# Kernel optimization log

Hardware: AMD Instinct MI355X
Metric: run time of the kernel (lower is better)

## Reference

```python
import jax, jax.numpy as jnp
import numpy as np


def setup_inputs() -> dict:
    key = jax.random.key(0)
    ks = jax.random.split(key, 6)
    B, S, D = 2048, 50, 128
    H, L = 8, 128
    return {
        "x": jax.random.normal(ks[0], (B, S, D), dtype=jnp.float32),
        "Wq": jax.random.normal(ks[1], (H, D, L), dtype=jnp.float32),
        "Wk": jax.random.normal(ks[2], (H, D, L), dtype=jnp.float32),
        "Wv": jax.random.normal(ks[3], (H, D, L), dtype=jnp.float32),
        "Ws": jax.random.normal(ks[4], (H, L), dtype=jnp.float32),
        "O": jax.random.normal(ks[5], (H * L, D), dtype=jnp.float32),
    }


def reference(x, Wq, Wk, Wv, Ws, O):
    # x: [B, S, D]; origin is the first node of each walk.
    B, S, D = x.shape
    H, _, L = Wq.shape
    origin = x[:, 0, :]  # [B, D]
    # key projection of origin is constant over the sequence -> compute once.
    k = jax.nn.sigmoid(jnp.einsum("bd,hdl->bhl", origin, Wk))  # [B, H, L]
    q = jax.nn.sigmoid(jnp.einsum("bsd,hdl->bshl", x, Wq))      # [B, S, H, L]
    v = jax.nn.sigmoid(jnp.einsum("bsd,hdl->bshl", x, Wv))      # [B, S, H, L]
    edge = k[:, None, :, :] * q                                  # [B, S, H, L]
    score = jnp.einsum("bshl,hl->bsh", edge, Ws)                 # [B, S, H]
    attn = jax.nn.softmax(score, axis=1)                         # softmax over walk positions
    res = jnp.einsum("bsh,bshl->bhl", attn, v)                   # [B, H, L]
    res = res.reshape(B, H * L)                                  # head-major concat (matches tf.concat)
    out = jax.nn.sigmoid(res @ O) + origin                       # [B, D]
    return out
```

## Files before the change

### kernel.cpp

```cpp
#include <hip/hip_runtime.h>
#include <hip/hip_bf16.h>


typedef _Float16 f16x8 __attribute__((ext_vector_type(8)));
typedef float f32x4 __attribute__((ext_vector_type(4)));

#define LOG2E 1.44269504088896340736f

__device__ __forceinline__ unsigned short f2h(float f) {
  _Float16 h = (_Float16)f;
  return __builtin_bit_cast(unsigned short, h);
}
__device__ __forceinline__ float h2f(unsigned short s) {
  return (float)__builtin_bit_cast(_Float16, s);
}
__device__ __forceinline__ float fexp2(float x) {
#if __has_builtin(__builtin_amdgcn_exp2f)
  return __builtin_amdgcn_exp2f(x);
#else
  return exp2f(x);
#endif
}
__device__ __forceinline__ float frcp(float x) {
#if __has_builtin(__builtin_amdgcn_rcpf)
  return __builtin_amdgcn_rcpf(x);
#else
  return 1.0f / x;
#endif
}
__device__ __forceinline__ float sig_scaled(float a) {
  return frcp(1.0f + fexp2(a));
}

__device__ __forceinline__ void dma16(const void* g, void* l) {
  __builtin_amdgcn_global_load_lds(
      (const __attribute__((address_space(1))) unsigned int*)g,
      (__attribute__((address_space(3))) unsigned int*)(unsigned int)(unsigned long long)l,
      16, 0, 0);
}

__global__ void prep_kernel(const float* __restrict__ Wq, const float* __restrict__ Wk,
                            const float* __restrict__ Wv, const float* __restrict__ O,
                            unsigned short* __restrict__ ws16) {
  const float NS = -LOG2E;
  int tid = blockIdx.x * 256 + threadIdx.x;
  for (int j = tid; j < 4 * 131072; j += 512 * 256) {
    int which = j >> 17;
    int i = j & 131071;
    float val;
    if (which == 0 || which == 2) {
      const float* W = (which == 0) ? Wq : Wv;
      int tau = i >> 11;
      int op = (i & 2047) * 2;
      int c = op >> 8;
      int o = op ^ ((c & 7) << 4);
      int k = (o & 255) >> 1;
      int n = tau * 16 + c;
      int h = n >> 7, lidx = n & 127;
      val = W[h * 16384 + k * 128 + lidx];
    } else if (which == 1) {
      int n = i >> 7, d = i & 127;
      int h = n >> 7, lidx = n & 127;
      val = Wk[h * 16384 + d * 128 + lidx];
    } else {
      int n = i >> 10, k = i & 1023;
      val = O[k * 128 + n];
    }
    ws16[j] = f2h(val * NS);
  }
}

__global__ __launch_bounds__(256, 2) void kw_kernel(
    const float* __restrict__ x, const float* __restrict__ Ws,
    const unsigned short* __restrict__ WkT, unsigned short* __restrict__ kw_all) {
  __shared__ __align__(16) char lds[8192];
  const int tid = threadIdx.x;
  const int b0 = blockIdx.x * 32;
  for (int i = tid; i < 1024; i += 256) {
    int row = i >> 5, c4 = i & 31;
    const float4 v = *(const float4*)(x + (size_t)(b0 + row) * 6400 + c4 * 4);
    uint2 pk;
    pk.x = (unsigned)f2h(v.x) | ((unsigned)f2h(v.y) << 16);
    pk.y = (unsigned)f2h(v.z) | ((unsigned)f2h(v.w) << 16);
    *(uint2*)(lds + row * 256 + ((c4 * 8) ^ ((row & 7) << 4))) = pk;
  }
  __syncthreads();
  const int w = tid >> 6, l = tid & 63, l15 = l & 15, l4 = l >> 4;
  f16x8 af[2][4];
#pragma unroll
  for (int mt = 0; mt < 2; ++mt)
#pragma unroll
    for (int kt = 0; kt < 4; ++kt) {
      int row = mt * 16 + l15;
      int c = kt * 64 + l4 * 16;
      af[mt][kt] = *(const f16x8*)(lds + row * 256 + (c ^ ((row & 7) << 4)));
    }
  const f16x8* B8 = (const f16x8*)WkT;
  for (int nt = 0; nt < 4; ++nt) {
    const int n0 = blockIdx.y * 256 + w * 64 + nt * 16;
    f16x8 bfr[4];
#pragma unroll
    for (int kt = 0; kt < 4; ++kt) bfr[kt] = B8[(size_t)(n0 + l15) * 16 + kt * 4 + l4];
    f32x4 acc[2];
#pragma unroll
    for (int mt = 0; mt < 2; ++mt) acc[mt] = (f32x4){0.f, 0.f, 0.f, 0.f};
#pragma unroll
    for (int mt = 0; mt < 2; ++mt)
#pragma unroll
      for (int kt = 0; kt < 4; ++kt)
        acc[mt] = __builtin_amdgcn_mfma_f32_16x16x32_f16(af[mt][kt], bfr[kt], acc[mt], 0, 0, 0);
    const float wsv = Ws[n0 + l15];
#pragma unroll
    for (int mt = 0; mt < 2; ++mt)
#pragma unroll
      for (int r = 0; r < 4; ++r) {
        int row = b0 + mt * 16 + l4 * 4 + r;
        kw_all[(size_t)row * 1024 + n0 + l15] = f2h(sig_scaled(acc[mt][r]) * wsv);
      }
  }
}

__global__ __launch_bounds__(256, 3) void fused_kernel(
    const float* __restrict__ x,
    const unsigned short* __restrict__ WqS, const unsigned short* __restrict__ WvS,
    const unsigned short* __restrict__ kw_all, unsigned short* __restrict__ res_all) {
  __shared__ __align__(16) char lds[49152];
  const int tid = threadIdx.x;
  const int b = blockIdx.x;
  const int w = tid >> 6, l = tid & 63, l15 = l & 15, l4 = l >> 4;
  const int ncol = w * 256;

  unsigned short kwr[16];
  {
    const unsigned short* kwp = kw_all + (size_t)b * 1024 + ncol + l15;
#pragma unroll
    for (int nt = 0; nt < 16; ++nt) kwr[nt] = kwp[nt * 16];
  }

  const float* xb = x + (size_t)b * 6400;
#pragma unroll
  for (int j = 0; j < 8; ++j) {
    int idx = tid + j * 256;
    int row = idx >> 5, c4 = idx & 31;
    uint2 pk = {0u, 0u};
    if (row < 50) {
      const float4 v = *(const float4*)(xb + row * 128 + c4 * 4);
      pk.x = (unsigned)f2h(v.x) | ((unsigned)f2h(v.y) << 16);
      pk.y = (unsigned)f2h(v.z) | ((unsigned)f2h(v.w) << 16);
    }
    *(uint2*)(lds + row * 256 + ((c4 * 8) ^ ((row & 7) << 4))) = pk;
  }
  __syncthreads();

  f16x8 af[4][4];
#pragma unroll
  for (int mt = 0; mt < 4; ++mt)
#pragma unroll
    for (int kt = 0; kt < 4; ++kt) {
      int row = mt * 16 + l15;
      int c = kt * 64 + l4 * 16;
      af[mt][kt] = *(const f16x8*)(lds + row * 256 + (c ^ ((row & 7) << 4)));
    }
  float kwf[16];
#pragma unroll
  for (int nt = 0; nt < 16; ++nt) kwf[nt] = h2f(kwr[nt]);
  __syncthreads();

  char* slotb = lds + w * 12288;

  {
    const char* s0 = (const char*)WqS + (size_t)(ncol >> 4) * 4096 + l * 16;
    dma16(s0, slotb);
    dma16(s0 + 1024, slotb + 1024);
    dma16(s0 + 2048, slotb + 2048);
    dma16(s0 + 3072, slotb + 3072);
    const char* s1 = s0 + 4096;
    char* n1 = slotb + 4096;
    dma16(s1, n1);
    dma16(s1 + 1024, n1 + 1024);
    dma16(s1 + 2048, n1 + 2048);
    dma16(s1 + 3072, n1 + 3072);
  }

  float pa[4][4];
#pragma unroll
  for (int mt = 0; mt < 4; ++mt)
#pragma unroll
    for (int r = 0; r < 4; ++r) pa[mt][r] = 0.f;

#pragma unroll
  for (int t = 0; t < 32; ++t) {
    const int nt = (t & 7) + ((t >> 4) << 3);
    char* cslot = slotb + (t % 3) * 4096;
    if (t < 30) {
      const int t2 = t + 2;
      const int nt2 = (t2 & 7) + ((t2 >> 4) << 3);
      const unsigned short* W2 = ((t2 >> 3) & 1) ? WvS : WqS;
      const char* s = (const char*)W2 + (size_t)((ncol >> 4) + nt2) * 4096 + l * 16;
      char* nslot = slotb + (t2 % 3) * 4096;
      dma16(s, nslot);
      dma16(s + 1024, nslot + 1024);
      dma16(s + 2048, nslot + 2048);
      dma16(s + 3072, nslot + 3072);
      asm volatile("s_waitcnt vmcnt(8)" ::: "memory");
    } else if (t == 30) {
      asm volatile("s_waitcnt vmcnt(4)" ::: "memory");
    } else {
      asm volatile("s_waitcnt vmcnt(0)" ::: "memory");
    }
    __builtin_amdgcn_s_setprio(1);
    f32x4 acc[4];
#pragma unroll
    for (int mt = 0; mt < 4; ++mt) acc[mt] = (f32x4){0.f, 0.f, 0.f, 0.f};
    {
      f16x8 bf0, bf1;
      {
        int o0 = (l15 * 256 + 0 * 64 + l4 * 16) ^ ((l15 & 7) << 4);
        int o1 = (l15 * 256 + 1 * 64 + l4 * 16) ^ ((l15 & 7) << 4);
        bf0 = *(const f16x8*)(cslot + o0);
        bf1 = *(const f16x8*)(cslot + o1);
      }
#pragma unroll
      for (int mt = 0; mt < 4; ++mt)
        acc[mt] = __builtin_amdgcn_mfma_f32_16x16x32_f16(af[mt][0], bf0, acc[mt], 0, 0, 0);
#pragma unroll
      for (int mt = 0; mt < 4; ++mt)
        acc[mt] = __builtin_amdgcn_mfma_f32_16x16x32_f16(af[mt][1], bf1, acc[mt], 0, 0, 0);
      {
        int o2 = (l15 * 256 + 2 * 64 + l4 * 16) ^ ((l15 & 7) << 4);
        int o3 = (l15 * 256 + 3 * 64 + l4 * 16) ^ ((l15 & 7) << 4);
        bf0 = *(const f16x8*)(cslot + o2);
        bf1 = *(const f16x8*)(cslot + o3);
      }
#pragma unroll
      for (int mt = 0; mt < 4; ++mt)
        acc[mt] = __builtin_amdgcn_mfma_f32_16x16x32_f16(af[mt][2], bf0, acc[mt], 0, 0, 0);
#pragma unroll
      for (int mt = 0; mt < 4; ++mt)
        acc[mt] = __builtin_amdgcn_mfma_f32_16x16x32_f16(af[mt][3], bf1, acc[mt], 0, 0, 0);
    }
    __builtin_amdgcn_s_setprio(0);

    if (((t >> 3) & 1) == 0) {
      const float kwv = kwf[nt];
#pragma unroll
      for (int mt = 0; mt < 4; ++mt)
#pragma unroll
        for (int r = 0; r < 4; ++r) {
          if (mt < 3 || r < 2)
            pa[mt][r] = fmaf(sig_scaled(acc[mt][r]), kwv, pa[mt][r]);
        }
      if ((t & 7) == 7) {
#pragma unroll
        for (int mt = 0; mt < 4; ++mt)
#pragma unroll
          for (int r = 0; r < 4; ++r) {
            if (mt == 3 && r >= 2) continue;
            float v = pa[mt][r];
            v += __shfl_xor(v, 1);
            v += __shfl_xor(v, 2);
            v += __shfl_xor(v, 4);
            v += __shfl_xor(v, 8);
            pa[mt][r] = v;
          }
        float m = -3.0e38f;
#pragma unroll
        for (int mt = 0; mt < 4; ++mt)
#pragma unroll
          for (int r = 0; r < 4; ++r) {
            if (mt == 3 && r >= 2) continue;
            int row = mt * 16 + l4 * 4 + r;
            m = fmaxf(m, (row < 50) ? pa[mt][r] : -3.0e38f);
          }
        m = fmaxf(m, __shfl_xor(m, 16));
        m = fmaxf(m, __shfl_xor(m, 32));
        float tsum = 0.f;
#pragma unroll
        for (int mt = 0; mt < 4; ++mt)
#pragma unroll
          for (int r = 0; r < 4; ++r) {
            int row = mt * 16 + l4 * 4 + r;
            float e = (row < 50 && !(mt == 3 && r >= 2))
                          ? fexp2((pa[mt][r] - m) * LOG2E) : 0.f;
            pa[mt][r] = e;
            tsum += e;
          }
        tsum += __shfl_xor(tsum, 16);
        tsum += __shfl_xor(tsum, 32);
        const float rs = frcp(tsum);
#pragma unroll
        for (int mt = 0; mt < 4; ++mt)
#pragma unroll
          for (int r = 0; r < 4; ++r) pa[mt][r] *= rs;
      }
    } else {
      float part = 0.f;
#pragma unroll
      for (int mt = 0; mt < 4; ++mt)
#pragma unroll
        for (int r = 0; r < 4; ++r) {
          if (mt < 3 || r < 2)
            part = fmaf(pa[mt][r], sig_scaled(acc[mt][r]), part);
        }
      part += __shfl_xor(part, 16);
      part += __shfl_xor(part, 32);
      if (l < 16)
        res_all[(size_t)b * 1024 + ncol + nt * 16 + l15] = f2h(part);
      if (t == 15) {
#pragma unroll
        for (int mt = 0; mt < 4; ++mt)
#pragma unroll
          for (int r = 0; r < 4; ++r) pa[mt][r] = 0.f;
      }
    }
  }
}

__global__ __launch_bounds__(256, 4) void out_kernel(
    const unsigned short* __restrict__ res_all, const unsigned short* __restrict__ OT,
    const float* __restrict__ x, float* __restrict__ out) {
  const int tid = threadIdx.x;
  const int w = tid >> 6, l = tid & 63, l15 = l & 15, l4 = l >> 4;
  const int b0 = blockIdx.x * 16;
  const int n0 = blockIdx.y * 64 + w * 16;
  const f16x8* A8 = (const f16x8*)res_all;
  const f16x8* B8 = (const f16x8*)OT;
  f32x4 acc = (f32x4){0.f, 0.f, 0.f, 0.f};
#pragma unroll 4
  for (int kt = 0; kt < 32; ++kt) {
    f16x8 a = A8[(size_t)(b0 + l15) * 128 + kt * 4 + l4];
    f16x8 bq = B8[(size_t)(n0 + l15) * 128 + kt * 4 + l4];
    acc = __builtin_amdgcn_mfma_f32_16x16x32_f16(a, bq, acc, 0, 0, 0);
  }
#pragma unroll
  for (int r = 0; r < 4; ++r) {
    int row = b0 + l4 * 4 + r;
    int col = n0 + l15;
    out[(size_t)row * 128 + col] = sig_scaled(acc[r]) + x[(size_t)row * 6400 + col];
  }
}

extern "C" void kernel_launch(void* const* d_in, const int* in_sizes, int n_in,
                              void* d_out, int out_size, void* d_ws, size_t ws_size,
                              hipStream_t stream) {
  const float* x  = (const float*)d_in[0];
  const float* Wq = (const float*)d_in[1];
  const float* Wk = (const float*)d_in[2];
  const float* Wv = (const float*)d_in[3];
  const float* Ws = (const float*)d_in[4];
  const float* O  = (const float*)d_in[5];
  float* out = (float*)d_out;

  unsigned short* ws16    = (unsigned short*)d_ws;
  unsigned short* WqS     = ws16;
  unsigned short* WkT     = ws16 + 131072;
  unsigned short* WvS     = ws16 + 262144;
  unsigned short* OT      = ws16 + 393216;
  unsigned short* kw_all  = ws16 + 524288;
  unsigned short* res_all = ws16 + 524288 + 2097152;

  prep_kernel<<<512, 256, 0, stream>>>(Wq, Wk, Wv, O, ws16);
  kw_kernel<<<dim3(64, 4), 256, 0, stream>>>(x, Ws, WkT, kw_all);
  fused_kernel<<<2048, 256, 0, stream>>>(x, WqS, WvS, kw_all, res_all);
  out_kernel<<<dim3(128, 2), 256, 0, stream>>>(res_all, OT, x, out);
}
```

Before: 117.3 us.

## Software-pipeline MFMA of next tile with epilogue of current tile

Restructures the fused kernel loop so the MFMA product for tile t+1 is issued before the sigmoid/softmax epilogue of tile t, ping-ponging between two accumulator sets. This lets matrix-core work overlap with the VALU/transcendental post-processing. The per-lane kw values now go into a small LDS array instead of 16 registers, which frees registers to hold the extra accumulators at the cost of an LDS read per tile. Wait counts on outstanding DMA are retuned for the shifted schedule.

```diff
diff --git a/kernel.cpp b/kernel.cpp
--- a/kernel.cpp
+++ b/kernel.cpp
@@ -125,17 +125,11 @@
     const unsigned short* __restrict__ WqS, const unsigned short* __restrict__ WvS,
     const unsigned short* __restrict__ kw_all, unsigned short* __restrict__ res_all) {
   __shared__ __align__(16) char lds[49152];
+  __shared__ __align__(16) unsigned short kw16[1024];
   const int tid = threadIdx.x;
   const int b = blockIdx.x;
   const int w = tid >> 6, l = tid & 63, l15 = l & 15, l4 = l >> 4;
   const int ncol = w * 256;
-
-  unsigned short kwr[16];
-  {
-    const unsigned short* kwp = kw_all + (size_t)b * 1024 + ncol + l15;
-#pragma unroll
-    for (int nt = 0; nt < 16; ++nt) kwr[nt] = kwp[nt * 16];
-  }
 
   const float* xb = x + (size_t)b * 6400;
 #pragma unroll
@@ -150,6 +144,8 @@
     }
     *(uint2*)(lds + row * 256 + ((c4 * 8) ^ ((row & 7) << 4))) = pk;
   }
+  *(ushort4*)(kw16 + tid * 4) =
+      *(const ushort4*)(kw_all + (size_t)b * 1024 + tid * 4);
   __syncthreads();
 
   f16x8 af[4][4];
@@ -161,12 +157,121 @@
       int c = kt * 64 + l4 * 16;
       af[mt][kt] = *(const f16x8*)(lds + row * 256 + (c ^ ((row & 7) << 4)));
     }
-  float kwf[16];
-#pragma unroll
-  for (int nt = 0; nt < 16; ++nt) kwf[nt] = h2f(kwr[nt]);
   __syncthreads();
 
   char* slotb = lds + w * 12288;
+
+  auto LDMFMA = [&](const char* cs, f32x4* acc) {
+#pragma unroll
+    for (int mt = 0; mt < 4; ++mt) acc[mt] = (f32x4){0.f, 0.f, 0.f, 0.f};
+    f16x8 bf0, bf1;
+    {
+      int o0 = (l15 * 256 + 0 * 64 + l4 * 16) ^ ((l15 & 7) << 4);
+      int o1 = (l15 * 256 + 1 * 64 + l4 * 16) ^ ((l15 & 7) << 4);
+      bf0 = *(const f16x8*)(cs + o0);
+      bf1 = *(const f16x8*)(cs + o1);
+    }
+#pragma unroll
+    for (int mt = 0; mt < 4; ++mt)
+      acc[mt] = __builtin_amdgcn_mfma_f32_16x16x32_f16(af[mt][0], bf0, acc[mt], 0, 0, 0);
+#pragma unroll
+    for (int mt = 0; mt < 4; ++mt)
+      acc[mt] = __builtin_amdgcn_mfma_f32_16x16x32_f16(af[mt][1], bf1, acc[mt], 0, 0, 0);
+    {
+      int o2 = (l15 * 256 + 2 * 64 + l4 * 16) ^ ((l15 & 7) << 4);
+      int o3 = (l15 * 256 + 3 * 64 + l4 * 16) ^ ((l15 & 7) << 4);
+      bf0 = *(const f16x8*)(cs + o2);
+      bf1 = *(const f16x8*)(cs + o3);
+    }
+#pragma unroll
+    for (int mt = 0; mt < 4; ++mt)
+      acc[mt] = __builtin_amdgcn_mfma_f32_16x16x32_f16(af[mt][2], bf0, acc[mt], 0, 0, 0);
+#pragma unroll
+    for (int mt = 0; mt < 4; ++mt)
+      acc[mt] = __builtin_amdgcn_mfma_f32_16x16x32_f16(af[mt][3], bf1, acc[mt], 0, 0, 0);
+  };
+
+  float pa[4][4];
+#pragma unroll
+  for (int mt = 0; mt < 4; ++mt)
+#pragma unroll
+    for (int r = 0; r < 4; ++r) pa[mt][r] = 0.f;
+
+  auto POST = [&](int t, f32x4* acc) {
+    const int nt = (t & 7) + ((t >> 4) << 3);
+    if (((t >> 3) & 1) == 0) {
+      const float kwv = h2f(kw16[ncol + nt * 16 + l15]);
+#pragma unroll
+      for (int mt = 0; mt < 4; ++mt)
+#pragma unroll
+        for (int r = 0; r < 4; ++r) {
+          if (mt < 3 || r < 2)
+            pa[mt][r] = fmaf(sig_scaled(acc[mt][r]), kwv, pa[mt][r]);
+        }
+      if ((t & 7) == 7) {
+#pragma unroll
+        for (int mt = 0; mt < 4; ++mt)
+#pragma unroll
+          for (int r = 0; r < 4; ++r) {
+            if (mt == 3 && r >= 2) continue;
+            float v = pa[mt][r];
+            v += __shfl_xor(v, 1);
+            v += __shfl_xor(v, 2);
+            v += __shfl_xor(v, 4);
+            v += __shfl_xor(v, 8);
+            pa[mt][r] = v;
+          }
+        float m = -3.0e38f;
+#pragma unroll
+        for (int mt = 0; mt < 4; ++mt)
+#pragma unroll
+          for (int r = 0; r < 4; ++r) {
+            if (mt == 3 && r >= 2) continue;
+            int row = mt * 16 + l4 * 4 + r;
+            m = fmaxf(m, (row < 50) ? pa[mt][r] : -3.0e38f);
+          }
+        m = fmaxf(m, __shfl_xor(m, 16));
+        m = fmaxf(m, __shfl_xor(m, 32));
+        float tsum = 0.f;
+#pragma unroll
+        for (int mt = 0; mt < 4; ++mt)
+#pragma unroll
+          for (int r = 0; r < 4; ++r) {
+            int row = mt * 16 + l4 * 4 + r;
+            float e = (row < 50 && !(mt == 3 && r >= 2))
+                          ? fexp2((pa[mt][r] - m) * LOG2E) : 0.f;
+            pa[mt][r] = e;
+            tsum += e;
+          }
+        tsum += __shfl_xor(tsum, 16);
+        tsum += __shfl_xor(tsum, 32);
+        const float rs = frcp(tsum);
+#pragma unroll
+        for (int mt = 0; mt < 4; ++mt)
+#pragma unroll
+          for (int r = 0; r < 4; ++r) pa[mt][r] *= rs;
+      }
+    } else {
+      float part = 0.f;
+#pragma unroll
+      for (int mt = 0; mt < 4; ++mt)
+#pragma unroll
+        for (int r = 0; r < 4; ++r) {
+          if (mt < 3 || r < 2)
+            part = fmaf(pa[mt][r], sig_scaled(acc[mt][r]), part);
+        }
+      part += __shfl_xor(part, 16);
+      part += __shfl_xor(part, 32);
+      if (l < 16)
+        res_all[(size_t)b * 1024 + ncol + nt * 16 + l15] = f2h(part);
+      if (t == 15) {
+#pragma unroll
+        for (int mt = 0; mt < 4; ++mt)
+#pragma unroll
+          for (int r = 0; r < 4; ++r) pa[mt][r] = 0.f;
+      }
+    }
+  };
 
   {
     const char* s0 = (const char*)WqS + (size_t)(ncol >> 4) * 4096 + l * 16;
@@ -181,18 +286,15 @@
     dma16(s1 + 2048, n1 + 2048);
     dma16(s1 + 3072, n1 + 3072);
   }
-
-  float pa[4][4];
-#pragma unroll
-  for (int mt = 0; mt < 4; ++mt)
-#pragma unroll
-    for (int r = 0; r < 4; ++r) pa[mt][r] = 0.f;
+  f32x4 accA[4], accB[4];
+  asm volatile("s_waitcnt vmcnt(4)" ::: "memory");
+  __builtin_amdgcn_s_setprio(1);
+  LDMFMA(slotb, accA);
+  __builtin_amdgcn_s_setprio(0);
 
 #pragma unroll
   for (int t = 0; t < 32; ++t) {
-    const int nt = (t & 7) + ((t >> 4) << 3);
-    char* cslot = slotb + (t % 3) * 4096;
-    if (t < 30) {
+    if (t + 2 < 32) {
       const int t2 = t + 2;
       const int nt2 = (t2 & 7) + ((t2 >> 4) << 3);
       const unsigned short* W2 = ((t2 >> 3) & 1) ? WvS : WqS;
@@ -202,117 +304,19 @@
       dma16(s + 1024, nslot + 1024);
       dma16(s + 2048, nslot + 2048);
       dma16(s + 3072, nslot + 3072);
-      asm volatile("s_waitcnt vmcnt(8)" ::: "memory");
-    } else if (t == 30) {
-      asm volatile("s_waitcnt vmcnt(4)" ::: "memory");
-    } else {
-      asm volatile("s_waitcnt vmcnt(0)" ::: "memory");
-    }
-    __builtin_amdgcn_s_setprio(1);
-    f32x4 acc[4];
-#pragma unroll
-    for (int mt = 0; mt < 4; ++mt) acc[mt] = (f32x4){0.f, 0.f, 0.f, 0.f};
-    {
-      f16x8 bf0, bf1;
-      {
-        int o0 = (l15 * 256 + 0 * 64 + l4 * 16) ^ ((l15 & 7) << 4);
-        int o1 = (l15 * 256 + 1 * 64 + l4 * 16) ^ ((l15 & 7) << 4);
-        bf0 = *(const f16x8*)(cslot + o0);
-        bf1 = *(const f16x8*)(cslot + o1);
+    }
+    if (t + 1 < 32) {
+      if (t + 2 < 32) {
+        asm volatile("s_waitcnt vmcnt(4)" ::: "memory");
+      } else {
+        asm volatile("s_waitcnt vmcnt(0)" ::: "memory");
       }
-#pragma unroll
-      for (int mt = 0; mt < 4; ++mt)
-        acc[mt] = __builtin_amdgcn_mfma_f32_16x16x32_f16(af[mt][0], bf0, acc[mt], 0, 0, 0);
-#pragma unroll
-      for (int mt = 0; mt < 4; ++mt)
-        acc[mt] = __builtin_amdgcn_mfma_f32_16x16x32_f16(af[mt][1], bf1, acc[mt], 0, 0, 0);
-      {
-        int o2 = (l15 * 256 + 2 * 64 + l4 * 16) ^ ((l15 & 7) << 4);
-        int o3 = (l15 * 256 + 3 * 64 + l4 * 16) ^ ((l15 & 7) << 4);
-        bf0 = *(const f16x8*)(cslot + o2);
-        bf1 = *(const f16x8*)(cslot + o3);
-      }
-#pragma unroll
-      for (int mt = 0; mt < 4; ++mt)
-        acc[mt] = __builtin_amdgcn_mfma_f32_16x16x32_f16(af[mt][2], bf0, acc[mt], 0, 0, 0);
-#pragma unroll
-      for (int mt = 0; mt < 4; ++mt)
-        acc[mt] = __builtin_amdgcn_mfma_f32_16x16x32_f16(af[mt][3], bf1, acc[mt], 0, 0, 0);
-    }
-    __builtin_amdgcn_s_setprio(0);
-
-    if (((t >> 3) & 1) == 0) {
-      const float kwv = kwf[nt];
-#pragma unroll
-      for (int mt = 0; mt < 4; ++mt)
-#pragma unroll
-        for (int r = 0; r < 4; ++r) {
-          if (mt < 3 || r < 2)
-            pa[mt][r] = fmaf(sig_scaled(acc[mt][r]), kwv, pa[mt][r]);
-        }
-      if ((t & 7) == 7) {
-#pragma unroll
-        for (int mt = 0; mt < 4; ++mt)
-#pragma unroll
-          for (int r = 0; r < 4; ++r) {
-            if (mt == 3 && r >= 2) continue;
-            float v = pa[mt][r];
-            v += __shfl_xor(v, 1);
-            v += __shfl_xor(v, 2);
-            v += __shfl_xor(v, 4);
-            v += __shfl_xor(v, 8);
-            pa[mt][r] = v;
-          }
-        float m = -3.0e38f;
-#pragma unroll
-        for (int mt = 0; mt < 4; ++mt)
-#pragma unroll
-          for (int r = 0; r < 4; ++r) {
-            if (mt == 3 && r >= 2) continue;
-            int row = mt * 16 + l4 * 4 + r;
-            m = fmaxf(m, (row < 50) ? pa[mt][r] : -3.0e38f);
-          }
-        m = fmaxf(m, __shfl_xor(m, 16));
-        m = fmaxf(m, __shfl_xor(m, 32));
-        float tsum = 0.f;
-#pragma unroll
-        for (int mt = 0; mt < 4; ++mt)
-#pragma unroll
-          for (int r = 0; r < 4; ++r) {
-            int row = mt * 16 + l4 * 4 + r;
-            float e = (row < 50 && !(mt == 3 && r >= 2))
-                          ? fexp2((pa[mt][r] - m) * LOG2E) : 0.f;
-            pa[mt][r] = e;
-            tsum += e;
-          }
-        tsum += __shfl_xor(tsum, 16);
-        tsum += __shfl_xor(tsum, 32);
-        const float rs = frcp(tsum);
-#pragma unroll
-        for (int mt = 0; mt < 4; ++mt)
-#pragma unroll
-          for (int r = 0; r < 4; ++r) pa[mt][r] *= rs;
-      }
-    } else {
-      float part = 0.f;
-#pragma unroll
-      for (int mt = 0; mt < 4; ++mt)
-#pragma unroll
-        for (int r = 0; r < 4; ++r) {
-          if (mt < 3 || r < 2)
-            part = fmaf(pa[mt][r], sig_scaled(acc[mt][r]), part);
-        }
-      part += __shfl_xor(part, 16);
-      part += __shfl_xor(part, 32);
-      if (l < 16)
-        res_all[(size_t)b * 1024 + ncol + nt * 16 + l15] = f2h(part);
-      if (t == 15) {
-#pragma unroll
-        for (int mt = 0; mt < 4; ++mt)
-#pragma unroll
-          for (int r = 0; r < 4; ++r) pa[mt][r] = 0.f;
-      }
-    }
+      const char* cs = slotb + ((t + 1) % 3) * 4096;
+      __builtin_amdgcn_s_setprio(1);
+      if (((t + 1) & 1) == 0) LDMFMA(cs, accA); else LDMFMA(cs, accB);
+      __builtin_amdgcn_s_setprio(0);
+    }
+    if ((t & 1) == 0) POST(t, accA); else POST(t, accB);
   }
 }
 
```

Measured after the change: 132.7 us. 1.13x slower.
